# Optimization experiments

Hardware: AMD Instinct MI355X
Metric: run time of the kernel (lower is better)

Reference implementation:

```python
import jax, jax.numpy as jnp
import numpy as np

B, N, IN_DIM, D, P, C = 256, 2048, 2, 128, 2048, 10
LN_EPS = 1e-5
NORM_EPS = 1e-12


def setup_inputs() -> dict:
    key = jax.random.key(0)
    ks = jax.random.split(key, 9)
    X = jax.random.normal(ks[0], (B, N, IN_DIM), dtype=jnp.float32)
    # deterministic pair subsample (stands in for torch.combinations + randperm[:max_pairs])
    rng = np.random.default_rng(0)
    i = rng.integers(0, N, size=(P,))
    j = rng.integers(0, N, size=(P,))
    j = np.where(i == j, (j + 1) % N, j)  # i != j, as combinations(r=2) guarantees
    pairs = jnp.asarray(np.stack([np.minimum(i, j), np.maximum(i, j)], axis=1), dtype=jnp.int32)
    # proj: Linear(2, D) + LayerNorm(D) (+ ReLU)
    W1 = jax.random.normal(ks[1], (IN_DIM, D), dtype=jnp.float32) / jnp.sqrt(jnp.float32(IN_DIM))
    b1 = jnp.zeros((D,), jnp.float32)
    gamma = jnp.ones((D,), jnp.float32)
    beta = jnp.zeros((D,), jnp.float32)
    # mlp: Linear(D, D) -> ReLU -> Linear(D, C)
    Wm1 = jax.random.normal(ks[2], (D, D), dtype=jnp.float32) / jnp.sqrt(jnp.float32(D))
    bm1 = jnp.zeros((D,), jnp.float32)
    Wm2 = jax.random.normal(ks[3], (D, C), dtype=jnp.float32) / jnp.sqrt(jnp.float32(D))
    bm2 = jnp.zeros((C,), jnp.float32)
    # frozen sdi_memory: row-normalized gaussian [C, D]
    mem = jax.random.normal(ks[4], (C, D), dtype=jnp.float32)
    mem = mem / jnp.maximum(jnp.linalg.norm(mem, axis=1, keepdims=True), NORM_EPS)
    return {"X": X, "pairs": pairs, "W1": W1, "b1": b1, "gamma": gamma, "beta": beta,
            "Wm1": Wm1, "bm1": bm1, "Wm2": Wm2, "bm2": bm2, "mem": mem}


def reference(X, pairs, W1, b1, gamma, beta, Wm1, bm1, Wm2, bm2, mem):
    # proj: Linear + LayerNorm (biased var, like torch) + ReLU  -> z: [B, N, D]
    h = jnp.einsum('bni,id->bnd', X, W1) + b1
    mu = h.mean(-1, keepdims=True)
    var = ((h - mu) ** 2).mean(-1, keepdims=True)
    z = jax.nn.relu(gamma * (h - mu) * jax.lax.rsqrt(var + LN_EPS) + beta)
    # pairwise gather: diffs then sums, concatenated along pair axis -> [B, 2P, D]
    za = z[:, pairs[:, 0], :]
    zb = z[:, pairs[:, 1], :]
    feats = jnp.concatenate([za - zb, za + zb], axis=1)
    # row-wise L2 normalize (F.normalize, eps=1e-12), then mean over pairs -> sdi: [B, D]
    feats = feats / jnp.maximum(jnp.linalg.norm(feats, axis=-1, keepdims=True), NORM_EPS)
    sdi = feats.mean(axis=1)
    # logits = sdi @ mem.T + mlp(sdi)
    logits = sdi @ mem.T + (jax.nn.relu(sdi @ Wm1 + bm1) @ Wm2 + bm2)
    return logits, sdi
```

## Files before the change

### kernel.cpp

```cpp
#include <hip/hip_runtime.h>

#define B 256
#define N 2048
#define P 2048
#define C 10
#define S_CHUNKS 4
#define PPB (P / S_CHUNKS)
#define NIT (PPB / 32)
#define LN_EPS 1e-5f

typedef float v2f __attribute__((ext_vector_type(2)));
typedef _Float16 h2 __attribute__((ext_vector_type(2)));

static __device__ __forceinline__ float fdot2(h2 a, h2 b, float c) {
#if __has_builtin(__builtin_amdgcn_fdot2)
    return __builtin_amdgcn_fdot2(a, b, c, false);
#else
    return (float)a.x * (float)b.x + (float)a.y * (float)b.y + c;
#endif
}
static __device__ __forceinline__ h2 h2fma(h2 a, h2 b, h2 c) {
#if __has_builtin(__builtin_elementwise_fma)
    return __builtin_elementwise_fma(a, b, c);
#else
    return a * b + c;
#endif
}
static __device__ __forceinline__ h2 h2relu(h2 x) {
#if __has_builtin(__builtin_elementwise_max)
    return __builtin_elementwise_max(x, h2{(_Float16)0.f, (_Float16)0.f});
#else
    h2 r;
    r.x = x.x > (_Float16)0.f ? x.x : (_Float16)0.f;
    r.y = x.y > (_Float16)0.f ? x.y : (_Float16)0.f;
    return r;
#endif
}
static __device__ __forceinline__ h2 pkrtz(float a, float b) {
#if __has_builtin(__builtin_amdgcn_cvt_pkrtz)
    return __builtin_bit_cast(h2, __builtin_amdgcn_cvt_pkrtz(a, b));
#else
    return h2{(_Float16)a, (_Float16)b};
#endif
}
static __device__ __forceinline__ unsigned pk_rne(float a, float b) {
    return __builtin_bit_cast(unsigned, h2{(_Float16)a, (_Float16)b});
}

static __device__ __forceinline__ float red16(float x) {
    x += __int_as_float(__builtin_amdgcn_update_dpp(0, __float_as_int(x), 0xB1,  0xF, 0xF, true));
    x += __int_as_float(__builtin_amdgcn_update_dpp(0, __float_as_int(x), 0x4E,  0xF, 0xF, true));
    x += __int_as_float(__builtin_amdgcn_update_dpp(0, __float_as_int(x), 0x141, 0xF, 0xF, true));
    x += __int_as_float(__builtin_amdgcn_update_dpp(0, __float_as_int(x), 0x140, 0xF, 0xF, true));
    return x;
}

__global__ __launch_bounds__(256) void fused_kernel(
        const float* __restrict__ X,
        const float* __restrict__ W1, const float* __restrict__ b1,
        const float* __restrict__ gamma, const float* __restrict__ beta,
        const int*   __restrict__ pairs,
        float* __restrict__ part) {
    const int b = blockIdx.x;
    const int chunk = blockIdx.y;
    const int tid = threadIdx.x;
    const int w = tid >> 6, l = tid & 63, g = l >> 4, s = l & 15;
    const int slot = w * 4 + g;

    __shared__ __align__(16) float lds[4096];
    __shared__ float wf[4][128];
    __shared__ float sc[9];
    uint2* Tl = (uint2*)lds;

    if (w == 0) {
        const float w0a = W1[l],       w0b = W1[l + 64];
        const float w1a = W1[128 + l], w1b = W1[128 + l + 64];
        const float bba = b1[l],       bbb = b1[l + 64];
        float s0 = w0a + w0b, s1 = w1a + w1b, sb = bba + bbb;
        #pragma unroll
        for (int m = 1; m < 64; m <<= 1) {
            s0 += __shfl_xor(s0, m);
            s1 += __shfl_xor(s1, m);
            sb += __shfl_xor(sb, m);
        }
        const float m0 = s0 * (1.f / 128.f);
        const float m1 = s1 * (1.f / 128.f);
        const float mb = sb * (1.f / 128.f);
        const float c0a = w0a - m0, c0b = w0b - m0;
        const float c1a = w1a - m1, c1b = w1b - m1;
        const float cba = bba - mb, cbb = bbb - mb;
        float q[6] = { c0a*c0a + c0b*c0b, c1a*c1a + c1b*c1b, cba*cba + cbb*cbb,
                       c0a*c1a + c0b*c1b, c0a*cba + c0b*cbb, c1a*cba + c1b*cbb };
        #pragma unroll
        for (int m = 1; m < 64; m <<= 1) {
            #pragma unroll
            for (int k = 0; k < 6; ++k) q[k] += __shfl_xor(q[k], m);
        }
        if (l < 6) sc[l] = q[l] * (1.f / 128.f);
        if (l == 6) sc[6] = m0;
        if (l == 7) sc[7] = m1;
        if (l == 8) sc[8] = mb;
    }
    __syncthreads();

    if (tid < 128) {
        const float m0 = sc[6], m1 = sc[7], mb = sc[8];
        const float g_ = gamma[tid];
        wf[0][tid] = g_ * (W1[tid] - m0);
        wf[1][tid] = g_ * (W1[128 + tid] - m1);
        wf[2][tid] = g_ * (b1[tid] - mb);
        wf[3][tid] = beta[tid];
    }

    {
        const float S00 = sc[0], S11 = sc[1], Sbb = sc[2];
        const float S01 = sc[3], S0b = sc[4], S1b = sc[5];
        const float2* Xb = (const float2*)(X + (size_t)b * N * 2);
        #pragma unroll
        for (int q = 0; q < 8; ++q) {
            const int n = q * 256 + tid;
            const float2 x = Xb[n];
            const float v = fmaf(x.x * x.x, S00, fmaf(x.y * x.y, S11, Sbb))
                          + 2.f * fmaf(x.x * x.y, S01, fmaf(x.x, S0b, x.y * S1b));
            const float rs = rsqrtf(v + LN_EPS);
            Tl[n] = uint2{pk_rne(rs * x.x, rs * x.y), pk_rne(rs, 1.f)};
        }
    }
    __syncthreads();

    h2 gw0[4], gw1[4], gbc[4], be2[4];
    #pragma unroll
    for (int m = 0; m < 4; ++m) {
        const int d0 = s + 32 * m, d1 = d0 + 16;
        gw0[m] = h2{(_Float16)wf[0][d0], (_Float16)wf[0][d1]};
        gw1[m] = h2{(_Float16)wf[1][d0], (_Float16)wf[1][d1]};
        gbc[m] = h2{(_Float16)wf[2][d0], (_Float16)wf[2][d1]};
        be2[m] = h2{(_Float16)wf[3][d0], (_Float16)wf[3][d1]};
    }

    const int4* pr4 = (const int4*)pairs;
    const int i4base = chunk * (PPB / 2);

    v2f acc[4];
    #pragma unroll
    for (int m = 0; m < 4; ++m) acc[m] = v2f{0.f, 0.f};

    auto proc = [&](const uint2 ti, const uint2 tj) {
        const h2 abi = __builtin_bit_cast(h2, ti.x), ci = __builtin_bit_cast(h2, ti.y);
        const h2 abj = __builtin_bit_cast(h2, tj.x), cj = __builtin_bit_cast(h2, tj.y);
        const h2 aai = h2{abi.x, abi.x}, bbi = h2{abi.y, abi.y}, cci = h2{ci.x, ci.x};
        const h2 aaj = h2{abj.x, abj.x}, bbj = h2{abj.y, abj.y}, ccj = h2{cj.x, cj.x};
        h2 uu[4], vv[4];
        float nu0 = 0.f, nu1 = 0.f, nv0 = 0.f, nv1 = 0.f;
        #pragma unroll
        for (int m = 0; m < 4; ++m) {
            const h2 hi = h2relu(h2fma(aai, gw0[m], h2fma(bbi, gw1[m], h2fma(cci, gbc[m], be2[m]))));
            const h2 hj = h2relu(h2fma(aaj, gw0[m], h2fma(bbj, gw1[m], h2fma(ccj, gbc[m], be2[m]))));
            const h2 u = hi - hj;
            const h2 v = hi + hj;
            if (m & 1) { nu1 = fdot2(u, u, nu1); nv1 = fdot2(v, v, nv1); }
            else       { nu0 = fdot2(u, u, nu0); nv0 = fdot2(v, v, nv0); }
            uu[m] = u; vv[m] = v;
        }
        const float nu = red16(nu0 + nu1);
        const float nv = red16(nv0 + nv1);
        const float ru = rsqrtf(fmaxf(nu, 1e-24f));
        const float rv = rsqrtf(fmaxf(nv, 1e-24f));
        const h2 ruv = pkrtz(ru, rv);
        #pragma unroll
        for (int m = 0; m < 4; ++m) {
            acc[m].x = fdot2(h2{uu[m].x, vv[m].x}, ruv, acc[m].x);
            acc[m].y = fdot2(h2{uu[m].y, vv[m].y}, ruv, acc[m].y);
        }
    };

    const int4 idx0 = pr4[i4base + slot];
    int4 idxN = pr4[i4base + 16 + slot];
    uint2 tiA = Tl[idx0.x], tjA = Tl[idx0.y];
    uint2 tiB = Tl[idx0.z], tjB = Tl[idx0.w];

    for (int t = 0; t < NIT; ++t) {
        const uint2 ntiA = Tl[idxN.x], ntjA = Tl[idxN.y];
        const uint2 ntiB = Tl[idxN.z], ntjB = Tl[idxN.w];
        const int t2 = (t + 2 < NIT) ? (t + 2) : (NIT - 1);
        const int4 idxNN = pr4[i4base + t2 * 16 + slot];

        proc(tiA, tjA);
        proc(tiB, tjB);

        tiA = ntiA; tjA = ntjA; tiB = ntiB; tjB = ntjB;
        idxN = idxNN;
    }

    __syncthreads();

    #pragma unroll
    for (int m = 0; m < 4; ++m) {
        lds[slot * 136 + (2 * m)     * 17 + s] = acc[m].x;
        lds[slot * 136 + (2 * m + 1) * 17 + s] = acc[m].y;
    }
    __syncthreads();
    if (tid < 128) {
        const int ss = tid & 15, kk = tid >> 4;
        float sum = 0.f;
        #pragma unroll
        for (int q = 0; q < 16; ++q) sum += lds[q * 136 + kk * 17 + ss];
        part[((size_t)b * S_CHUNKS + chunk) * 128 + tid] = sum;
    }
}

__global__ __launch_bounds__(256) void head_kernel(
        const float* __restrict__ part,
        const float* __restrict__ Wm1, const float* __restrict__ bm1,
        const float* __restrict__ Wm2, const float* __restrict__ bm2,
        const float* __restrict__ mem,
        float* __restrict__ out_logits, float* __restrict__ out_sdi) {
    const int b = blockIdx.x;
    const int t = threadIdx.x;
    __shared__ float s[128];
    __shared__ float h[128];

    if (t < 128) {
        float sv = 0.f;
        #pragma unroll
        for (int k = 0; k < S_CHUNKS; ++k)
            sv += part[((size_t)b * S_CHUNKS + k) * 128 + t];
        sv *= (1.f / (2.f * P));
        s[t] = sv;
        out_sdi[(size_t)b * 128 + t] = sv;
    }
    __syncthreads();
    if (t < 128) {
        float a = bm1[t];
        for (int d = 0; d < 128; ++d) a = fmaf(s[d], Wm1[d * 128 + t], a);
        h[t] = fmaxf(a, 0.f);
    }
    __syncthreads();
    if (t < 16 * C) {
        const int c = t >> 4, l = t & 15;
        float lg = 0.f;
        #pragma unroll
        for (int q = 0; q < 8; ++q) {
            const int d = l + 16 * q;
            lg = fmaf(s[d], mem[c * 128 + d], fmaf(h[d], Wm2[d * C + c], lg));
        }
        lg = red16(lg);
        if (l == 0) out_logits[(size_t)b * C + c] = lg + bm2[c];
    }
}

extern "C" void kernel_launch(void* const* d_in, const int* in_sizes, int n_in,
                              void* d_out, int out_size, void* d_ws, size_t ws_size,
                              hipStream_t stream) {
    const float* X     = (const float*)d_in[0];
    const int*   pairs = (const int*)  d_in[1];
    const float* W1    = (const float*)d_in[2];
    const float* b1    = (const float*)d_in[3];
    const float* gamma = (const float*)d_in[4];
    const float* beta  = (const float*)d_in[5];
    const float* Wm1   = (const float*)d_in[6];
    const float* bm1   = (const float*)d_in[7];
    const float* Wm2   = (const float*)d_in[8];
    const float* bm2   = (const float*)d_in[9];
    const float* mem   = (const float*)d_in[10];

    float* out = (float*)d_out;
    float* part = (float*)d_ws;

    fused_kernel<<<dim3(B, S_CHUNKS), 256, 0, stream>>>(X, W1, b1, gamma, beta,
                                                        pairs, part);
    head_kernel<<<B, 256, 0, stream>>>(part, Wm1, bm1, Wm2, bm2, mem,
                                       out, out + (size_t)B * C);
}
```

Before: 32.36 us.

## Fuse head into main kernel via last-block atomic counter; widen per-lane D slice

The separate head kernel is removed. Each chunk block increments a per-batch atomic counter after writing its partial sums, and the last block to arrive computes sdi and the MLP and memory logits, which saves one kernel launch. The pair loop also changes from 16 lanes per pair with 8 feature elements each to 8 lanes per pair with 16 elements each, so twice as many pairs run in parallel, the norm reduction is shorter, and register use roughly doubles. A hipMemsetAsync is added to reset the counters, which places an extra operation on the stream.

```diff
diff --git a/kernel.cpp b/kernel.cpp
--- a/kernel.cpp
+++ b/kernel.cpp
@@ -6,7 +6,7 @@
 #define C 10
 #define S_CHUNKS 4
 #define PPB (P / S_CHUNKS)
-#define NIT (PPB / 32)
+#define NIT (PPB / 64)
 #define LN_EPS 1e-5f
 
 typedef float v2f __attribute__((ext_vector_type(2)));
@@ -47,10 +47,14 @@
     return __builtin_bit_cast(unsigned, h2{(_Float16)a, (_Float16)b});
 }
 
-static __device__ __forceinline__ float red16(float x) {
+static __device__ __forceinline__ float red8(float x) {
     x += __int_as_float(__builtin_amdgcn_update_dpp(0, __float_as_int(x), 0xB1,  0xF, 0xF, true));
     x += __int_as_float(__builtin_amdgcn_update_dpp(0, __float_as_int(x), 0x4E,  0xF, 0xF, true));
     x += __int_as_float(__builtin_amdgcn_update_dpp(0, __float_as_int(x), 0x141, 0xF, 0xF, true));
+    return x;
+}
+static __device__ __forceinline__ float red16(float x) {
+    x = red8(x);
     x += __int_as_float(__builtin_amdgcn_update_dpp(0, __float_as_int(x), 0x140, 0xF, 0xF, true));
     return x;
 }
@@ -60,16 +64,22 @@
         const float* __restrict__ W1, const float* __restrict__ b1,
         const float* __restrict__ gamma, const float* __restrict__ beta,
         const int*   __restrict__ pairs,
-        float* __restrict__ part) {
+        const float* __restrict__ Wm1, const float* __restrict__ bm1,
+        const float* __restrict__ Wm2, const float* __restrict__ bm2,
+        const float* __restrict__ mem,
+        float* __restrict__ part, int* __restrict__ cnt,
+        float* __restrict__ out_logits, float* __restrict__ out_sdi) {
     const int b = blockIdx.x;
     const int chunk = blockIdx.y;
     const int tid = threadIdx.x;
-    const int w = tid >> 6, l = tid & 63, g = l >> 4, s = l & 15;
-    const int slot = w * 4 + g;
+    const int w = tid >> 6, l = tid & 63, g = l >> 3, s = l & 7;
+    const int slot = w * 8 + g;
 
     __shared__ __align__(16) float lds[4096];
+    __shared__ __align__(16) float scr[32 * 129];
     __shared__ float wf[4][128];
     __shared__ float sc[9];
+    __shared__ int lastFlag;
     uint2* Tl = (uint2*)lds;
 
     if (w == 0) {
@@ -128,10 +138,10 @@
     }
     __syncthreads();
 
-    h2 gw0[4], gw1[4], gbc[4], be2[4];
+    h2 gw0[8], gw1[8], gbc[8], be2[8];
     #pragma unroll
-    for (int m = 0; m < 4; ++m) {
-        const int d0 = s + 32 * m, d1 = d0 + 16;
+    for (int m = 0; m < 8; ++m) {
+        const int d0 = s + 16 * m, d1 = d0 + 8;
         gw0[m] = h2{(_Float16)wf[0][d0], (_Float16)wf[0][d1]};
         gw1[m] = h2{(_Float16)wf[1][d0], (_Float16)wf[1][d1]};
         gbc[m] = h2{(_Float16)wf[2][d0], (_Float16)wf[2][d1]};
@@ -141,19 +151,19 @@
     const int4* pr4 = (const int4*)pairs;
     const int i4base = chunk * (PPB / 2);
 
-    v2f acc[4];
+    v2f acc[8];
     #pragma unroll
-    for (int m = 0; m < 4; ++m) acc[m] = v2f{0.f, 0.f};
+    for (int m = 0; m < 8; ++m) acc[m] = v2f{0.f, 0.f};
 
     auto proc = [&](const uint2 ti, const uint2 tj) {
         const h2 abi = __builtin_bit_cast(h2, ti.x), ci = __builtin_bit_cast(h2, ti.y);
         const h2 abj = __builtin_bit_cast(h2, tj.x), cj = __builtin_bit_cast(h2, tj.y);
         const h2 aai = h2{abi.x, abi.x}, bbi = h2{abi.y, abi.y}, cci = h2{ci.x, ci.x};
         const h2 aaj = h2{abj.x, abj.x}, bbj = h2{abj.y, abj.y}, ccj = h2{cj.x, cj.x};
-        h2 uu[4], vv[4];
+        h2 uu[8], vv[8];
         float nu0 = 0.f, nu1 = 0.f, nv0 = 0.f, nv1 = 0.f;
         #pragma unroll
-        for (int m = 0; m < 4; ++m) {
+        for (int m = 0; m < 8; ++m) {
             const h2 hi = h2relu(h2fma(aai, gw0[m], h2fma(bbi, gw1[m], h2fma(cci, gbc[m], be2[m]))));
             const h2 hj = h2relu(h2fma(aaj, gw0[m], h2fma(bbj, gw1[m], h2fma(ccj, gbc[m], be2[m]))));
             const h2 u = hi - hj;
@@ -162,20 +172,20 @@
             else       { nu0 = fdot2(u, u, nu0); nv0 = fdot2(v, v, nv0); }
             uu[m] = u; vv[m] = v;
         }
-        const float nu = red16(nu0 + nu1);
-        const float nv = red16(nv0 + nv1);
+        const float nu = red8(nu0 + nu1);
+        const float nv = red8(nv0 + nv1);
         const float ru = rsqrtf(fmaxf(nu, 1e-24f));
         const float rv = rsqrtf(fmaxf(nv, 1e-24f));
         const h2 ruv = pkrtz(ru, rv);
         #pragma unroll
-        for (int m = 0; m < 4; ++m) {
+        for (int m = 0; m < 8; ++m) {
             acc[m].x = fdot2(h2{uu[m].x, vv[m].x}, ruv, acc[m].x);
             acc[m].y = fdot2(h2{uu[m].y, vv[m].y}, ruv, acc[m].y);
         }
     };
 
     const int4 idx0 = pr4[i4base + slot];
-    int4 idxN = pr4[i4base + 16 + slot];
+    int4 idxN = pr4[i4base + 32 + slot];
     uint2 tiA = Tl[idx0.x], tjA = Tl[idx0.y];
     uint2 tiB = Tl[idx0.z], tjB = Tl[idx0.w];
 
@@ -183,7 +193,7 @@
         const uint2 ntiA = Tl[idxN.x], ntjA = Tl[idxN.y];
         const uint2 ntiB = Tl[idxN.z], ntjB = Tl[idxN.w];
         const int t2 = (t + 2 < NIT) ? (t + 2) : (NIT - 1);
-        const int4 idxNN = pr4[i4base + t2 * 16 + slot];
+        const int4 idxNN = pr4[i4base + t2 * 32 + slot];
 
         proc(tiA, tjA);
         proc(tiB, tjB);
@@ -192,60 +202,56 @@
         idxN = idxNN;
     }
 
-    __syncthreads();
-
     #pragma unroll
-    for (int m = 0; m < 4; ++m) {
-        lds[slot * 136 + (2 * m)     * 17 + s] = acc[m].x;
-        lds[slot * 136 + (2 * m + 1) * 17 + s] = acc[m].y;
-    }
-    __syncthreads();
-    if (tid < 128) {
-        const int ss = tid & 15, kk = tid >> 4;
+    for (int m = 0; m < 8; ++m) {
+        scr[slot * 129 + (2 * m)     * 8 + s] = acc[m].x;
+        scr[slot * 129 + (2 * m + 1) * 8 + s] = acc[m].y;
+    }
+    __syncthreads();
+    if (tid < 128) {
         float sum = 0.f;
         #pragma unroll
-        for (int q = 0; q < 16; ++q) sum += lds[q * 136 + kk * 17 + ss];
+        for (int q = 0; q < 32; ++q) sum += scr[q * 129 + tid];
         part[((size_t)b * S_CHUNKS + chunk) * 128 + tid] = sum;
     }
-}
-
-__global__ __launch_bounds__(256) void head_kernel(
-        const float* __restrict__ part,
-        const float* __restrict__ Wm1, const float* __restrict__ bm1,
-        const float* __restrict__ Wm2, const float* __restrict__ bm2,
-        const float* __restrict__ mem,
-        float* __restrict__ out_logits, float* __restrict__ out_sdi) {
-    const int b = blockIdx.x;
-    const int t = threadIdx.x;
-    __shared__ float s[128];
-    __shared__ float h[128];
-
-    if (t < 128) {
+
+    __threadfence();
+    if (tid == 0) {
+        const int old = atomicAdd(&cnt[b], 1);
+        lastFlag = (old == S_CHUNKS - 1);
+    }
+    __syncthreads();
+    if (!lastFlag) return;
+    __threadfence();
+
+    float* sA = wf[0];
+    float* hA = wf[1];
+    if (tid < 128) {
         float sv = 0.f;
         #pragma unroll
         for (int k = 0; k < S_CHUNKS; ++k)
-            sv += part[((size_t)b * S_CHUNKS + k) * 128 + t];
+            sv += part[((size_t)b * S_CHUNKS + k) * 128 + tid];
         sv *= (1.f / (2.f * P));
-        s[t] = sv;
-        out_sdi[(size_t)b * 128 + t] = sv;
-    }
-    __syncthreads();
-    if (t < 128) {
-        float a = bm1[t];
-        for (int d = 0; d < 128; ++d) a = fmaf(s[d], Wm1[d * 128 + t], a);
-        h[t] = fmaxf(a, 0.f);
-    }
-    __syncthreads();
-    if (t < 16 * C) {
-        const int c = t >> 4, l = t & 15;
+        sA[tid] = sv;
+        out_sdi[(size_t)b * 128 + tid] = sv;
+    }
+    __syncthreads();
+    if (tid < 128) {
+        float a = bm1[tid];
+        for (int d = 0; d < 128; ++d) a = fmaf(sA[d], Wm1[d * 128 + tid], a);
+        hA[tid] = fmaxf(a, 0.f);
+    }
+    __syncthreads();
+    if (tid < 16 * C) {
+        const int c = tid >> 4, l16 = tid & 15;
         float lg = 0.f;
         #pragma unroll
         for (int q = 0; q < 8; ++q) {
-            const int d = l + 16 * q;
-            lg = fmaf(s[d], mem[c * 128 + d], fmaf(h[d], Wm2[d * C + c], lg));
+            const int d = l16 + 16 * q;
+            lg = fmaf(sA[d], mem[c * 128 + d], fmaf(hA[d], Wm2[d * C + c], lg));
         }
         lg = red16(lg);
-        if (l == 0) out_logits[(size_t)b * C + c] = lg + bm2[c];
+        if (l16 == 0) out_logits[(size_t)b * C + c] = lg + bm2[c];
     }
 }
 
@@ -264,11 +270,14 @@
     const float* bm2   = (const float*)d_in[9];
     const float* mem   = (const float*)d_in[10];
 
-    float* out = (float*)d_out;
+    float* out_logits = (float*)d_out;
+    float* out_sdi    = (float*)d_out + (size_t)B * C;
     float* part = (float*)d_ws;
-
-    fused_kernel<<<dim3(B, S_CHUNKS), 256, 0, stream>>>(X, W1, b1, gamma, beta,
-                                                        pairs, part);
-    head_kernel<<<B, 256, 0, stream>>>(part, Wm1, bm1, Wm2, bm2, mem,
-                                       out, out + (size_t)B * C);
-}
+    int*   cnt  = (int*)((float*)d_ws + (size_t)B * S_CHUNKS * 128);
+
+    hipMemsetAsync(cnt, 0, B * sizeof(int), stream);
+
+    fused_kernel<<<dim3(B, S_CHUNKS), 256, 0, stream>>>(
+        X, W1, b1, gamma, beta, pairs, Wm1, bm1, Wm2, bm2, mem,
+        part, cnt, out_logits, out_sdi);
+}
```

After: 97.84 us. 3.02x slower.
